# Kernel optimization log

Hardware: AMD Instinct MI355X
Metric: run time of the kernel (lower is better)

Reference implementation:

```python
import jax, jax.numpy as jnp
import numpy as np

T = 524288
INPUT_LEN = 64
N_MEMORY = 64
OUTPUT_LEN = 32


def setup_inputs() -> dict:
    key = jax.random.key(0)
    k_x, k_w1, k_b1, k_w2, k_b2 = jax.random.split(key, 5)
    s = 0.05  # tf.random_normal_initializer default stddev
    return {
        "inputs": jax.random.normal(k_x, (T, INPUT_LEN), dtype=jnp.float32),
        "W1": s * jax.random.normal(k_w1, (INPUT_LEN, 2 * N_MEMORY), dtype=jnp.float32),
        "B1": s * jax.random.normal(k_b1, (1, 2 * N_MEMORY), dtype=jnp.float32),
        "W2": s * jax.random.normal(k_w2, (N_MEMORY, OUTPUT_LEN), dtype=jnp.float32),
        "B2": s * jax.random.normal(k_b2, (1, OUTPUT_LEN), dtype=jnp.float32),
    }


def reference(inputs, W1, B1, W2, B2):
    n_memory = W2.shape[0]
    # gates: h = sigmoid(x W1 + B1), split into left/right halves  [T, M] each
    h = jax.nn.sigmoid(inputs @ W1 + B1)
    left, right = jnp.split(h, 2, axis=1)
    prod = left * right
    # affine linear recurrence: u_t = prod_{t-1} * u_{t-1} + (1 - left_{t-1}), u_0 = 0
    a = prod[:-1]            # [T-1, M] multiplicative coeffs
    b = 1.0 - left[:-1]      # [T-1, M] additive terms

    def step(u, ab):
        a_t, b_t = ab
        u = a_t * u + b_t
        return u, u

    u0 = jnp.zeros((n_memory,), dtype=inputs.dtype)
    _, us = jax.lax.scan(step, u0, (a, b))
    z = jnp.concatenate([u0[None, :], us], axis=0)  # [T, M]
    out = z @ W2 + B2                               # [T, output_len]
    return out
```

## Files before the change

kernel.cpp:

```cpp
#include <hip/hip_runtime.h>

#define TT    524288
#define CHUNK 512
#define NCH   (TT / CHUNK)
#define SUB   64
#define NSUB  (CHUNK / SUB)

typedef __attribute__((ext_vector_type(8))) short short8;
typedef __attribute__((ext_vector_type(4))) float f32x4;

__device__ __forceinline__ unsigned short f2bf(float f) {
    union { float f; unsigned u; } v; v.f = f;
    unsigned r = v.u + 0x7FFFu + ((v.u >> 16) & 1u);
    return (unsigned short)(r >> 16);
}
__device__ __forceinline__ unsigned packbf2(float a, float b) {
    union { float f; unsigned u; } va, vb; va.f = a; vb.f = b;
    unsigned ra = va.u + 0x7FFFu + ((va.u >> 16) & 1u);
    unsigned rb = vb.u + 0x7FFFu + ((vb.u >> 16) & 1u);
    return (ra >> 16) | (rb & 0xFFFF0000u);
}
__device__ __forceinline__ float2 unpackbf2(unsigned w) {
    union { unsigned u; float f; } a, b;
    a.u = w << 16; b.u = w & 0xFFFF0000u;
    return make_float2(a.f, b.f);
}
__device__ __forceinline__ float sigf(float v) {
    return __builtin_amdgcn_rcpf(1.0f + __expf(-v));
}

union U8 { uint4 u4; short8 s8; };

__global__ __launch_bounds__(256, 3)
void aphase(const float* __restrict__ x, const float* __restrict__ W1,
            const float* __restrict__ B1,
            float* __restrict__ Aout, float* __restrict__ Bout,
            uint4* __restrict__ abg)
{
    __shared__ __align__(16) short W1t[128 * 72];
    __shared__ float    B1s[128];
    __shared__ unsigned abw[4][16 * 66];
    __shared__ float    segA[32 * 66], segB[32 * 66];

    const int tid  = threadIdx.x;
    const int c    = blockIdx.x;
    const int wave = tid >> 6;
    const int lane = tid & 63;
    const int quad = lane >> 4;
    const int lr   = lane & 15;

    for (int i = tid; i < 2048; i += 256) {
        float4 w4 = ((const float4*)W1)[i];
        int k = i >> 5, n0 = (i & 31) * 4;
        W1t[(n0 + 0) * 72 + k] = (short)f2bf(w4.x);
        W1t[(n0 + 1) * 72 + k] = (short)f2bf(w4.y);
        W1t[(n0 + 2) * 72 + k] = (short)f2bf(w4.z);
        W1t[(n0 + 3) * 72 + k] = (short)f2bf(w4.w);
    }
    if (tid < 128) B1s[tid] = B1[tid];
    __syncthreads();

    float bb[8];
    #pragma unroll
    for (int j = 0; j < 8; ++j) bb[j] = B1s[j * 16 + lr];

    const float* xbase = x + (size_t)c * CHUNK * 64;

    #define FRAGP(ss, rt) ((const float4*)(xbase + (size_t)(((ss) * 64 + (rt) * 16 + lr)) * 64) + quad * 2)

    const float4* p0 = FRAGP(wave, 0);
    float4 c0 = p0[0], c1 = p0[1], c2 = p0[8], c3 = p0[9];

    for (int fi = 0; fi < 8; ++fi) {
        const int ss = (fi < 4) ? wave : (wave + 4);
        const int rt = fi & 3;

        float4 n0, n1, n2, n3;
        if (fi < 7) {
            const int ns = (fi + 1 < 4) ? wave : (wave + 4);
            const int nr = (fi + 1) & 3;
            const float4* np = FRAGP(ns, nr);
            n0 = np[0]; n1 = np[1]; n2 = np[8]; n3 = np[9];
        }

        U8 ua, ub;
        ua.u4 = make_uint4(packbf2(c0.x, c0.y), packbf2(c0.z, c0.w),
                           packbf2(c1.x, c1.y), packbf2(c1.z, c1.w));
        ub.u4 = make_uint4(packbf2(c2.x, c2.y), packbf2(c2.z, c2.w),
                           packbf2(c3.x, c3.y), packbf2(c3.z, c3.w));
        const short8 a0 = ua.s8, a1 = ub.s8;

        f32x4 acc[8];
        #pragma unroll
        for (int j = 0; j < 8; ++j) {
            acc[j][0] = bb[j]; acc[j][1] = bb[j]; acc[j][2] = bb[j]; acc[j][3] = bb[j];
        }
        #pragma unroll
        for (int j = 0; j < 8; ++j) {
            const short8 b0 = *(const short8*)&W1t[(j * 16 + lr) * 72 + quad * 8];
            const short8 b1 = *(const short8*)&W1t[(j * 16 + lr) * 72 + quad * 8 + 32];
            acc[j] = __builtin_amdgcn_mfma_f32_16x16x32_bf16(a0, b0, acc[j], 0, 0, 0);
            acc[j] = __builtin_amdgcn_mfma_f32_16x16x32_bf16(a1, b1, acc[j], 0, 0, 0);
        }

        unsigned pk[4][4];
        #pragma unroll
        for (int j = 0; j < 4; ++j) {
            #pragma unroll
            for (int r = 0; r < 4; ++r) {
                float hl = sigf(acc[j][r]);
                float hr = sigf(acc[j + 4][r]);
                pk[j][r] = packbf2(hl * hr, 1.0f - hl);
            }
        }

        {
            uint4* dstq = abg + ((size_t)((c * NSUB + ss) * 16 + rt * 4 + quad)) * 64 + lr;
            #pragma unroll
            for (int j = 0; j < 4; ++j)
                dstq[j * 16] = make_uint4(pk[j][0], pk[j][1], pk[j][2], pk[j][3]);
        }

        #pragma unroll
        for (int j = 0; j < 4; ++j) {
            #pragma unroll
            for (int r = 0; r < 4; ++r)
                abw[wave][(quad * 4 + r) * 66 + j * 16 + lr] = pk[j][r];
        }
        float A = 1.0f, Bv = 0.0f;
        #pragma unroll
        for (int t = 0; t < 16; ++t) {
            float2 f2 = unpackbf2(abw[wave][t * 66 + lane]);
            Bv = fmaf(f2.x, Bv, f2.y); A *= f2.x;
        }
        const int band = ss * 4 + rt;
        segA[band * 66 + lane] = A;
        segB[band * 66 + lane] = Bv;

        if (fi < 7) { c0 = n0; c1 = n1; c2 = n2; c3 = n3; }
    }
    #undef FRAGP

    __syncthreads();
    if (tid < 64) {
        float sA = 1.0f, sB = 0.0f;
        for (int b = 0; b < 32; ++b) {
            float A2 = segA[b * 66 + tid], B2v = segB[b * 66 + tid];
            sB = fmaf(A2, sB, B2v); sA *= A2;
        }
        Aout[c * 64 + tid] = sA; Bout[c * 64 + tid] = sB;
    }
}

__global__ void carry_scan(const float* __restrict__ Aar, const float* __restrict__ Bar,
                           float* __restrict__ carry)
{
    __shared__ float sA[16 * 66], sB[16 * 66];
    const int tid = threadIdx.x;
    const int ch = tid & 63, seg = tid >> 6;
    const int c0 = seg * (NCH / 16);

    float A = 1.0f, B = 0.0f;
    #pragma unroll 8
    for (int i = 0; i < NCH / 16; ++i) {
        const int idx = c0 + i;
        const float a = Aar[idx * 64 + ch];
        const float b = Bar[idx * 64 + ch];
        B = fmaf(a, B, b); A *= a;
    }
    sA[seg * 66 + ch] = A;
    sB[seg * 66 + ch] = B;
    __syncthreads();

    float u = 0.0f;
    #pragma unroll
    for (int q = 0; q < 15; ++q)
        if (q < seg) u = fmaf(sA[q * 66 + ch], u, sB[q * 66 + ch]);
    #pragma unroll 8
    for (int i = 0; i < NCH / 16; ++i) {
        const int idx = c0 + i;
        carry[idx * 64 + ch] = u;
        u = fmaf(Aar[idx * 64 + ch], u, Bar[idx * 64 + ch]);
    }
}

__global__ __launch_bounds__(256, 4)
void ephase(const uint4* __restrict__ abg, const float* __restrict__ carry,
            const float* __restrict__ W2, const float* __restrict__ B2,
            float* __restrict__ out)
{
    __shared__ __align__(16) short Zs[SUB * 72];
    __shared__ float segA[2 * 4 * 66], segB[2 * 4 * 66];
    __shared__ __align__(16) short W2t[32 * 72];
    __shared__ float B2s[32];
    __shared__ float ucur[2 * 64];

    const int tid  = threadIdx.x;
    const int c    = blockIdx.x;
    const int wave = tid >> 6;
    const int lane = tid & 63;
    const int quad = lane >> 4;
    const int lr   = lane & 15;

    for (int i = tid; i < 512; i += 256) {
        float4 w4 = ((const float4*)W2)[i];
        int k = i >> 3, n0 = (i & 7) * 4;
        W2t[(n0 + 0) * 72 + k] = (short)f2bf(w4.x);
        W2t[(n0 + 1) * 72 + k] = (short)f2bf(w4.y);
        W2t[(n0 + 2) * 72 + k] = (short)f2bf(w4.z);
        W2t[(n0 + 3) * 72 + k] = (short)f2bf(w4.w);
    }
    if (tid < 32) B2s[tid] = B2[tid];
    if (tid < 64) ucur[tid] = carry[c * 64 + tid];

    const uint4* ag = abg + (size_t)c * (NSUB * 16 * 64);
    uint4 r0 = ag[(wave * 4 + 0) * 64 + lane];
    uint4 r1 = ag[(wave * 4 + 1) * 64 + lane];
    uint4 r2 = ag[(wave * 4 + 2) * 64 + lane];
    uint4 r3 = ag[(wave * 4 + 3) * 64 + lane];

    for (int s = 0; s < NSUB; ++s) {
        const int pb = (s & 1) * 264;

        uint4 n0, n1, n2, n3;
        if (s + 1 < NSUB) {
            const uint4* an = ag + (size_t)(s + 1) * (16 * 64);
            n0 = an[(wave * 4 + 0) * 64 + lane];
            n1 = an[(wave * 4 + 1) * 64 + lane];
            n2 = an[(wave * 4 + 2) * 64 + lane];
            n3 = an[(wave * 4 + 3) * 64 + lane];
        }

        float A = 1.0f, Bv = 0.0f; float2 f;
#define CSTEP(W) { f = unpackbf2(W); Bv = fmaf(f.x, Bv, f.y); A *= f.x; }
        CSTEP(r0.x) CSTEP(r0.y) CSTEP(r0.z) CSTEP(r0.w)
        CSTEP(r1.x) CSTEP(r1.y) CSTEP(r1.z) CSTEP(r1.w)
        CSTEP(r2.x) CSTEP(r2.y) CSTEP(r2.z) CSTEP(r2.w)
        CSTEP(r3.x) CSTEP(r3.y) CSTEP(r3.z) CSTEP(r3.w)
#undef CSTEP
        segA[pb + wave * 66 + lane] = A;
        segB[pb + wave * 66 + lane] = Bv;
        __syncthreads();

        float u = ucur[(s & 1) * 64 + lane];
        #pragma unroll
        for (int q = 0; q < 3; ++q)
            if (q < wave) u = fmaf(segA[pb + q * 66 + lane], u, segB[pb + q * 66 + lane]);

        int t = 0;
#define ESTEP(W) { Zs[(wave * 16 + t) * 72 + lane] = (short)f2bf(u); \
                   f = unpackbf2(W); u = fmaf(f.x, u, f.y); ++t; }
        ESTEP(r0.x) ESTEP(r0.y) ESTEP(r0.z) ESTEP(r0.w)
        ESTEP(r1.x) ESTEP(r1.y) ESTEP(r1.z) ESTEP(r1.w)
        ESTEP(r2.x) ESTEP(r2.y) ESTEP(r2.z) ESTEP(r2.w)
        ESTEP(r3.x) ESTEP(r3.y) ESTEP(r3.z) ESTEP(r3.w)
#undef ESTEP
        if (wave == 3) ucur[((s + 1) & 1) * 64 + lane] = u;

        const short8 za0 = *(const short8*)&Zs[(wave * 16 + lr) * 72 + quad * 8];
        const short8 za1 = *(const short8*)&Zs[(wave * 16 + lr) * 72 + quad * 8 + 32];
        const size_t row0g = (size_t)c * CHUNK + (size_t)s * SUB;
        #pragma unroll
        for (int nt = 0; nt < 2; ++nt) {
            f32x4 cc;
            float b = B2s[nt * 16 + lr];
            cc[0] = b; cc[1] = b; cc[2] = b; cc[3] = b;
            const short8 b0 = *(const short8*)&W2t[(nt * 16 + lr) * 72 + quad * 8];
            const short8 b1 = *(const short8*)&W2t[(nt * 16 + lr) * 72 + quad * 8 + 32];
            cc = __builtin_amdgcn_mfma_f32_16x16x32_bf16(za0, b0, cc, 0, 0, 0);
            cc = __builtin_amdgcn_mfma_f32_16x16x32_bf16(za1, b1, cc, 0, 0, 0);
            #pragma unroll
            for (int r = 0; r < 4; ++r) {
                int m = wave * 16 + quad * 4 + r;
                out[(row0g + m) * 32 + nt * 16 + lr] = cc[r];
            }
        }
        if (s + 1 < NSUB) { r0 = n0; r1 = n1; r2 = n2; r3 = n3; }
    }
}

extern "C" void kernel_launch(void* const* d_in, const int* in_sizes, int n_in,
                              void* d_out, int out_size, void* d_ws, size_t ws_size,
                              hipStream_t stream)
{
    const float* x  = (const float*)d_in[0];
    const float* W1 = (const float*)d_in[1];
    const float* B1 = (const float*)d_in[2];
    const float* W2 = (const float*)d_in[3];
    const float* B2 = (const float*)d_in[4];
    float* out = (float*)d_out;

    float* Aar   = (float*)d_ws;
    float* Bar   = Aar + NCH * 64;
    float* carry = Bar + NCH * 64;
    uint4* abg   = (uint4*)(carry + NCH * 64);

    aphase<<<NCH, 256, 0, stream>>>(x, W1, B1, Aar, Bar, abg);
    carry_scan<<<1, 1024, 0, stream>>>(Aar, Bar, carry);
    ephase<<<NCH, 256, 0, stream>>>(abg, carry, W2, B2, out);
}
```

Before: 302.6 us.

## Replace LDS transpose scan with wave shuffles and raise occupancy in both phases

In aphase, the per-16-row segment scan no longer goes through an LDS transpose buffer (abw). Each lane first composes its own four rows, then combines across quads with two xor-shuffle steps, which removes that shared memory and its round trip. Launch bounds go up (aphase 3→4, ephase 4→6), and ephase now issues the next sub-block's loads after the serial scan rather than holding double-buffered registers. This trades a shorter explicit prefetch distance for lower register pressure and higher occupancy.

```diff
diff --git a/kernel.cpp b/kernel.cpp
--- a/kernel.cpp
+++ b/kernel.cpp
@@ -31,7 +31,7 @@
 
 union U8 { uint4 u4; short8 s8; };
 
-__global__ __launch_bounds__(256, 3)
+__global__ __launch_bounds__(256, 4)
 void aphase(const float* __restrict__ x, const float* __restrict__ W1,
             const float* __restrict__ B1,
             float* __restrict__ Aout, float* __restrict__ Bout,
@@ -39,7 +39,6 @@
 {
     __shared__ __align__(16) short W1t[128 * 72];
     __shared__ float    B1s[128];
-    __shared__ unsigned abw[4][16 * 66];
     __shared__ float    segA[32 * 66], segB[32 * 66];
 
     const int tid  = threadIdx.x;
@@ -71,6 +70,9 @@
     const float4* p0 = FRAGP(wave, 0);
     float4 c0 = p0[0], c1 = p0[1], c2 = p0[8], c3 = p0[9];
 
+    const bool h1 = (quad & 1) != 0;
+    const bool h2 = (quad & 2) != 0;
+
     for (int fi = 0; fi < 8; ++fi) {
         const int ss = (fi < 4) ? wave : (wave + 4);
         const int rt = fi & 3;
@@ -121,21 +123,42 @@
                 dstq[j * 16] = make_uint4(pk[j][0], pk[j][1], pk[j][2], pk[j][3]);
         }
 
+        float Aa[4], Ba[4];
         #pragma unroll
         for (int j = 0; j < 4; ++j) {
+            float A = 1.0f, Bv = 0.0f;
             #pragma unroll
-            for (int r = 0; r < 4; ++r)
-                abw[wave][(quad * 4 + r) * 66 + j * 16 + lr] = pk[j][r];
-        }
-        float A = 1.0f, Bv = 0.0f;
-        #pragma unroll
-        for (int t = 0; t < 16; ++t) {
-            float2 f2 = unpackbf2(abw[wave][t * 66 + lane]);
-            Bv = fmaf(f2.x, Bv, f2.y); A *= f2.x;
-        }
+            for (int r = 0; r < 4; ++r) {
+                float2 f = unpackbf2(pk[j][r]);
+                Bv = fmaf(f.x, Bv, f.y); A *= f.x;
+            }
+            Aa[j] = A; Ba[j] = Bv;
+        }
+        #pragma unroll
+        for (int j = 0; j < 4; ++j) {
+            float Ap = __shfl_xor(Aa[j], 16);
+            float Bp = __shfl_xor(Ba[j], 16);
+            float Ahi = h1 ? Aa[j] : Ap;
+            float Blo = h1 ? Bp    : Ba[j];
+            float Bhi = h1 ? Ba[j] : Bp;
+            Aa[j] *= Ap;
+            Ba[j] = fmaf(Ahi, Blo, Bhi);
+
+            Ap = __shfl_xor(Aa[j], 32);
+            Bp = __shfl_xor(Ba[j], 32);
+            Ahi = h2 ? Aa[j] : Ap;
+            Blo = h2 ? Bp    : Ba[j];
+            Bhi = h2 ? Ba[j] : Bp;
+            Aa[j] *= Ap;
+            Ba[j] = fmaf(Ahi, Blo, Bhi);
+        }
+        const float Asel = (quad == 0) ? Aa[0] : (quad == 1) ? Aa[1]
+                         : (quad == 2) ? Aa[2] : Aa[3];
+        const float Bsel = (quad == 0) ? Ba[0] : (quad == 1) ? Ba[1]
+                         : (quad == 2) ? Ba[2] : Ba[3];
         const int band = ss * 4 + rt;
-        segA[band * 66 + lane] = A;
-        segB[band * 66 + lane] = Bv;
+        segA[band * 66 + lane] = Asel;
+        segB[band * 66 + lane] = Bsel;
 
         if (fi < 7) { c0 = n0; c1 = n1; c2 = n2; c3 = n3; }
     }
@@ -184,7 +207,7 @@
     }
 }
 
-__global__ __launch_bounds__(256, 4)
+__global__ __launch_bounds__(256, 6)
 void ephase(const uint4* __restrict__ abg, const float* __restrict__ carry,
             const float* __restrict__ W2, const float* __restrict__ B2,
             float* __restrict__ out)
@@ -221,15 +244,6 @@
 
     for (int s = 0; s < NSUB; ++s) {
         const int pb = (s & 1) * 264;
-
-        uint4 n0, n1, n2, n3;
-        if (s + 1 < NSUB) {
-            const uint4* an = ag + (size_t)(s + 1) * (16 * 64);
-            n0 = an[(wave * 4 + 0) * 64 + lane];
-            n1 = an[(wave * 4 + 1) * 64 + lane];
-            n2 = an[(wave * 4 + 2) * 64 + lane];
-            n3 = an[(wave * 4 + 3) * 64 + lane];
-        }
 
         float A = 1.0f, Bv = 0.0f; float2 f;
 #define CSTEP(W) { f = unpackbf2(W); Bv = fmaf(f.x, Bv, f.y); A *= f.x; }
@@ -256,6 +270,14 @@
         ESTEP(r3.x) ESTEP(r3.y) ESTEP(r3.z) ESTEP(r3.w)
 #undef ESTEP
         if (wave == 3) ucur[((s + 1) & 1) * 64 + lane] = u;
+
+        if (s + 1 < NSUB) {
+            const uint4* an = ag + (size_t)(s + 1) * (16 * 64);
+            r0 = an[(wave * 4 + 0) * 64 + lane];
+            r1 = an[(wave * 4 + 1) * 64 + lane];
+            r2 = an[(wave * 4 + 2) * 64 + lane];
+            r3 = an[(wave * 4 + 3) * 64 + lane];
+        }
 
         const short8 za0 = *(const short8*)&Zs[(wave * 16 + lr) * 72 + quad * 8];
         const short8 za1 = *(const short8*)&Zs[(wave * 16 + lr) * 72 + quad * 8 + 32];
@@ -275,7 +297,6 @@
                 out[(row0g + m) * 32 + nt * 16 + lr] = cc[r];
             }
         }
-        if (s + 1 < NSUB) { r0 = n0; r1 = n1; r2 = n2; r3 = n3; }
     }
 }
 
```

New measurement: 326.7 us. 1.08x slower.
